# Kernel tuning notes

Measured on AMD Instinct MI355X. Metric: run time of the kernel, lower is better.

## Reference

```python
import jax, jax.numpy as jnp
import numpy as np

IGNORE_INDEX = -100


def setup_inputs() -> dict:
    key = jax.random.key(0)
    k1, k2, k3 = jax.random.split(key, 3)
    VOCAB, D = 32000, 2048
    B, S = 4, 2048
    weight = jax.random.normal(k1, (VOCAB, D), dtype=jnp.float32) * 0.02
    hidden = jax.random.normal(k2, (B, S, D), dtype=jnp.float32)
    targets = jax.random.randint(k3, (B, S), 0, VOCAB, dtype=jnp.int64)
    return {"weight": weight, "hidden": hidden, "targets": targets}


def reference(weight, hidden, targets):
    # Fused linear + cross-entropy: loss = sum_t CE(hidden_t @ W^T, target_t) / n_valid.
    # (The torch module chunks over sequence purely to save memory; the math is
    # identical to the unchunked computation below.)
    B, S, D = hidden.shape
    flat_h = hidden.reshape(-1, D)            # [B*S, D]
    flat_t = targets.reshape(-1)              # [B*S]
    logits = (flat_h @ weight.T).astype(jnp.float32)  # [B*S, V]
    lse = jax.nn.logsumexp(logits, axis=-1)   # [B*S]
    safe_t = jnp.clip(flat_t, 0, logits.shape[-1] - 1)
    tgt_logit = jnp.take_along_axis(logits, safe_t[:, None], axis=-1)[:, 0]
    valid = flat_t != IGNORE_INDEX
    per_tok = jnp.where(valid, lse - tgt_logit, 0.0)
    total_loss = per_tok.sum()
    n_valid = valid.sum().astype(jnp.float32)
    return jnp.where(n_valid > 0, total_loss / n_valid, total_loss)
```

## Files before the change

kernel.cpp:

```cpp
#include <hip/hip_runtime.h>

#define IGNORE_INDEX (-100)
#define VOCAB 32000
#define DDIM  2048
#define MTOK  8192

#define BM 128
#define BN 128
#define BK 128

#define WSCALE 32.0f
#define HSCALE 8.0f
#define INVSCALE (1.0f / 256.0f)
#define SCALE_ONE 0x7F7F7F7F

#define WBLK ((VOCAB * DDIM) / (256 * 16))
#define HBLK ((MTOK * DDIM) / (256 * 16))

typedef float f32x4 __attribute__((ext_vector_type(4)));
typedef int   i32x8 __attribute__((ext_vector_type(8)));
typedef unsigned char uchar_t;

__device__ __forceinline__ void cvt16(const float4* __restrict__ src,
                                      int4* __restrict__ dst, float scale,
                                      size_t i) {
    float4 a = src[4 * i], b = src[4 * i + 1], c = src[4 * i + 2], d = src[4 * i + 3];
    int4 o;
    int v;
    v = 0;
    v = __builtin_amdgcn_cvt_pk_fp8_f32(a.x * scale, a.y * scale, v, false);
    v = __builtin_amdgcn_cvt_pk_fp8_f32(a.z * scale, a.w * scale, v, true);
    o.x = v;
    v = 0;
    v = __builtin_amdgcn_cvt_pk_fp8_f32(b.x * scale, b.y * scale, v, false);
    v = __builtin_amdgcn_cvt_pk_fp8_f32(b.z * scale, b.w * scale, v, true);
    o.y = v;
    v = 0;
    v = __builtin_amdgcn_cvt_pk_fp8_f32(c.x * scale, c.y * scale, v, false);
    v = __builtin_amdgcn_cvt_pk_fp8_f32(c.z * scale, c.w * scale, v, true);
    o.z = v;
    v = 0;
    v = __builtin_amdgcn_cvt_pk_fp8_f32(d.x * scale, d.y * scale, v, false);
    v = __builtin_amdgcn_cvt_pk_fp8_f32(d.z * scale, d.w * scale, v, true);
    o.w = v;
    dst[i] = o;
}

__global__ void cvt_f32_fp8(const float4* __restrict__ srcW, int4* __restrict__ dstW,
                            const float4* __restrict__ srcH, int4* __restrict__ dstH) {
    if (blockIdx.x < WBLK) {
        size_t i = (size_t)blockIdx.x * blockDim.x + threadIdx.x;
        cvt16(srcW, dstW, WSCALE, i);
    } else {
        size_t i = (size_t)(blockIdx.x - WBLK) * blockDim.x + threadIdx.x;
        cvt16(srcH, dstH, HSCALE, i);
    }
}

__device__ __forceinline__ void load_lds16(const uchar_t* g, uchar_t* l) {
    __builtin_amdgcn_global_load_lds(
        (const __attribute__((address_space(1))) unsigned int*)(const void*)g,
        (__attribute__((address_space(3))) unsigned int*)(void*)l,
        16, 0, 0);
}

__global__ __launch_bounds__(256, 4) void gemm_ce(
    const uchar_t* __restrict__ A,
    const uchar_t* __restrict__ B,
    const int* __restrict__ targets,
    float* __restrict__ sumexp,
    float* __restrict__ tgtlogit) {
    __shared__ alignas(16) uchar_t As[BM * BK];
    __shared__ alignas(16) uchar_t Bs[BN * BK];

    const int tid  = threadIdx.x;
    const int wave = tid >> 6;
    const int lane = tid & 63;
    const int quad = lane >> 4;
    const int l16  = lane & 15;
    const int wm   = (wave >> 1) * 64;
    const int wn   = (wave & 1) * 64;

    const int m0 = blockIdx.x * BM;
    const int n0 = blockIdx.y * BN;

    const int srow = lane >> 3;
    const int scol = ((((lane & 7) >> 1) ^ (srow & 3)) << 5) + ((lane & 1) << 4);

    const uchar_t* Ap = A + (size_t)(m0 + wave * 32 + srow) * DDIM + scol;
    const uchar_t* Bp = B + (size_t)(n0 + wave * 32 + srow) * DDIM + scol;
    uchar_t* AsW = &As[(wave * 32) * BK];
    uchar_t* BsW = &Bs[(wave * 32) * BK];

    f32x4 acc[4][4];
    const f32x4 zero = {0.f, 0.f, 0.f, 0.f};
#pragma unroll
    for (int i = 0; i < 4; ++i)
#pragma unroll
        for (int j = 0; j < 4; ++j) acc[i][j] = zero;

#pragma clang loop unroll(disable)
    for (int k0 = 0; k0 < DDIM; k0 += BK) {
#pragma unroll
        for (int it = 0; it < 4; ++it) {
            load_lds16(Ap + (size_t)it * 8 * DDIM + k0, AsW + it * 8 * BK);
            load_lds16(Bp + (size_t)it * 8 * DDIM + k0, BsW + it * 8 * BK);
        }
        __syncthreads();

        const int gsw = ((quad ^ (l16 & 3)) << 5);
        i32x8 af[4];
#pragma unroll
        for (int i = 0; i < 4; ++i)
            af[i] = *reinterpret_cast<const i32x8*>(
                &As[(wm + i * 16 + l16) * BK + gsw]);
#pragma unroll
        for (int j = 0; j < 4; ++j) {
            const i32x8 bf = *reinterpret_cast<const i32x8*>(
                &Bs[(wn + j * 16 + l16) * BK + gsw]);
#pragma unroll
            for (int i = 0; i < 4; ++i)
                acc[i][j] = __builtin_amdgcn_mfma_scale_f32_16x16x128_f8f6f4(
                    af[i], bf, acc[i][j],
                    0 , 0 ,
                    0, SCALE_ONE, 0, SCALE_ONE);
        }
        __syncthreads();
    }

#pragma unroll
    for (int i = 0; i < 4; ++i) {
#pragma unroll
        for (int r = 0; r < 4; ++r) {
            const int mg = m0 + wm + i * 16 + quad * 4 + r;
            const int t  = targets[mg];
            float p = 0.f;
#pragma unroll
            for (int j = 0; j < 4; ++j) {
                float v = acc[i][j][r] * INVSCALE;
                p += __expf(v);
                if (t == n0 + wn + j * 16 + l16) tgtlogit[mg] = v;
            }
            p += __shfl_xor(p, 1);
            p += __shfl_xor(p, 2);
            p += __shfl_xor(p, 4);
            p += __shfl_xor(p, 8);
            if (l16 == 0) atomicAdd(&sumexp[mg], p);
        }
    }
}

__global__ void finalize(const float* __restrict__ sumexp,
                         const float* __restrict__ tgtlogit,
                         const int* __restrict__ targets,
                         float* __restrict__ out) {
    __shared__ float s_sum[8];
    __shared__ float s_cnt[8];
    float local = 0.f, cnt = 0.f;
    for (int t = threadIdx.x; t < MTOK; t += blockDim.x) {
        int tg = targets[t];
        if (tg != IGNORE_INDEX) {
            local += logf(sumexp[t]) - tgtlogit[t];
            cnt += 1.f;
        }
    }
#pragma unroll
    for (int o = 32; o > 0; o >>= 1) {
        local += __shfl_down(local, o);
        cnt   += __shfl_down(cnt, o);
    }
    const int wave = threadIdx.x >> 6, lane = threadIdx.x & 63;
    if (lane == 0) { s_sum[wave] = local; s_cnt[wave] = cnt; }
    __syncthreads();
    if (threadIdx.x == 0) {
        float ts = 0.f, tc = 0.f;
        for (int w = 0; w < (int)(blockDim.x >> 6); ++w) {
            ts += s_sum[w];
            tc += s_cnt[w];
        }
        out[0] = (tc > 0.f) ? (ts / tc) : ts;
    }
}

extern "C" void kernel_launch(void* const* d_in, const int* in_sizes, int n_in,
                              void* d_out, int out_size, void* d_ws,
                              size_t ws_size, hipStream_t stream) {
    const float* weight  = (const float*)d_in[0];
    const float* hidden  = (const float*)d_in[1];
    const int*   targets = (const int*)d_in[2];
    float* out = (float*)d_out;

    const size_t wbytes = (size_t)VOCAB * DDIM;
    const size_t hbytes = (size_t)MTOK * DDIM;
    uchar_t* Wb = (uchar_t*)d_ws;
    uchar_t* Hb = (uchar_t*)d_ws + wbytes;
    float* sumexp   = (float*)((char*)d_ws + wbytes + hbytes);
    float* tgtlogit = sumexp + MTOK;

    cvt_f32_fp8<<<WBLK + HBLK, 256, 0, stream>>>(
        (const float4*)weight, (int4*)Wb, (const float4*)hidden, (int4*)Hb);

    hipMemsetAsync(sumexp, 0, 2 * MTOK * sizeof(float), stream);

    dim3 grid(MTOK / BM, VOCAB / BN);
    gemm_ce<<<grid, 256, 0, stream>>>(Hb, Wb, targets, sumexp, tgtlogit);

    finalize<<<1, 512, 0, stream>>>(sumexp, tgtlogit, targets, out);
}
```

Baseline: 975.2 us.

## Enlarge GEMM tiles to 256x256 with double-buffered LDS and interleaved prefetch

Raises the block tile to 256x256 with 8 waves (each wave 128x64) and double-buffers the LDS, interleaving global-to-LDS prefetch of the next K tile with MFMA groups under s_setprio and explicit barriers. It also pre-reduces the per-row sum-of-exp across waves in LDS before a single atomic per row, and folds the workspace zeroing into the conversion kernel instead of a separate memset. The intent is more data reuse per loaded byte, hidden global latency, fewer atomics and one fewer launch. The trade-off is 128 KB of LDS per block, which caps occupancy at 1 block per CU despite the launch_bounds of 2, plus higher register pressure from 32 accumulators.

```diff
diff --git a/kernel.cpp b/kernel.cpp
--- a/kernel.cpp
+++ b/kernel.cpp
@@ -5,9 +5,10 @@
 #define DDIM  2048
 #define MTOK  8192
 
-#define BM 128
-#define BN 128
+#define BM 256
+#define BN 256
 #define BK 128
+#define NKT (DDIM / BK)
 
 #define WSCALE 32.0f
 #define HSCALE 8.0f
@@ -16,6 +17,7 @@
 
 #define WBLK ((VOCAB * DDIM) / (256 * 16))
 #define HBLK ((MTOK * DDIM) / (256 * 16))
+#define ZBLK ((2 * MTOK * 4) / (256 * 16))
 
 typedef float f32x4 __attribute__((ext_vector_type(4)));
 typedef int   i32x8 __attribute__((ext_vector_type(8)));
@@ -47,13 +49,17 @@
 }
 
 __global__ void cvt_f32_fp8(const float4* __restrict__ srcW, int4* __restrict__ dstW,
-                            const float4* __restrict__ srcH, int4* __restrict__ dstH) {
+                            const float4* __restrict__ srcH, int4* __restrict__ dstH,
+                            int4* __restrict__ zr) {
     if (blockIdx.x < WBLK) {
         size_t i = (size_t)blockIdx.x * blockDim.x + threadIdx.x;
         cvt16(srcW, dstW, WSCALE, i);
-    } else {
+    } else if (blockIdx.x < WBLK + HBLK) {
         size_t i = (size_t)(blockIdx.x - WBLK) * blockDim.x + threadIdx.x;
         cvt16(srcH, dstH, HSCALE, i);
+    } else {
+        int i = (blockIdx.x - WBLK - HBLK) * 256 + threadIdx.x;
+        zr[i] = make_int4(0, 0, 0, 0);
     }
 }
 
@@ -64,75 +70,135 @@
         16, 0, 0);
 }
 
-__global__ __launch_bounds__(256, 4) void gemm_ce(
+__device__ __forceinline__ i32x8 read_frag(const uchar_t* arr, int off) {
+    int4 lo = *reinterpret_cast<const int4*>(arr + off);
+    int4 hi = *reinterpret_cast<const int4*>(arr + (off ^ 16));
+    i32x8 r;
+    r[0] = lo.x; r[1] = lo.y; r[2] = lo.z; r[3] = lo.w;
+    r[4] = hi.x; r[5] = hi.y; r[6] = hi.z; r[7] = hi.w;
+    return r;
+}
+
+__global__ __launch_bounds__(512, 2) void gemm_ce(
     const uchar_t* __restrict__ A,
     const uchar_t* __restrict__ B,
     const int* __restrict__ targets,
     float* __restrict__ sumexp,
     float* __restrict__ tgtlogit) {
-    __shared__ alignas(16) uchar_t As[BM * BK];
-    __shared__ alignas(16) uchar_t Bs[BN * BK];
+    __shared__ alignas(16) uchar_t As[2][BM * BK];
+    __shared__ alignas(16) uchar_t Bs[2][BN * BK];
 
     const int tid  = threadIdx.x;
     const int wave = tid >> 6;
     const int lane = tid & 63;
     const int quad = lane >> 4;
     const int l16  = lane & 15;
-    const int wm   = (wave >> 1) * 64;
-    const int wn   = (wave & 1) * 64;
+    const int wm   = (wave >> 2) * 128;
+    const int wn   = (wave & 3) * 64;
 
     const int m0 = blockIdx.x * BM;
     const int n0 = blockIdx.y * BN;
 
     const int srow = lane >> 3;
-    const int scol = ((((lane & 7) >> 1) ^ (srow & 3)) << 5) + ((lane & 1) << 4);
-
-    const uchar_t* Ap = A + (size_t)(m0 + wave * 32 + srow) * DDIM + scol;
-    const uchar_t* Bp = B + (size_t)(n0 + wave * 32 + srow) * DDIM + scol;
-    uchar_t* AsW = &As[(wave * 32) * BK];
-    uchar_t* BsW = &Bs[(wave * 32) * BK];
-
-    f32x4 acc[4][4];
+    const int sswz = ((lane & 7) ^ srow) << 4;
+    const uchar_t* Ag = A + (size_t)(m0 + wave * 8 + srow) * DDIM + sswz;
+    const uchar_t* Bg = B + (size_t)(n0 + wave * 8 + srow) * DDIM + sswz;
+
+    const int swlo = ((quad << 1) ^ (l16 & 7)) << 4;
+    const int aoff = (wm + l16) * BK + swlo;
+    const int boff = (wn + l16) * BK + swlo;
+
+    f32x4 acc[8][4];
     const f32x4 zero = {0.f, 0.f, 0.f, 0.f};
 #pragma unroll
-    for (int i = 0; i < 4; ++i)
+    for (int i = 0; i < 8; ++i)
 #pragma unroll
         for (int j = 0; j < 4; ++j) acc[i][j] = zero;
 
+#define STAGE_A(nb, it, k0) \
+    load_lds16(Ag + (size_t)(it) * 64 * DDIM + (k0), &As[nb][(it) * 8192 + wave * 1024])
+#define STAGE_B(nb, it, k0) \
+    load_lds16(Bg + (size_t)(it) * 64 * DDIM + (k0), &Bs[nb][(it) * 8192 + wave * 1024])
+#define LGKM0 asm volatile("s_waitcnt lgkmcnt(0)" ::: "memory")
+#define VM0   asm volatile("s_waitcnt vmcnt(0)" ::: "memory")
+#define BAR   __builtin_amdgcn_s_barrier()
+
+#define MFMA_PAIR(I0)                                                          \
+    _Pragma("unroll") for (int j = 0; j < 4; ++j) {                            \
+        acc[(I0)][j] = __builtin_amdgcn_mfma_scale_f32_16x16x128_f8f6f4(       \
+            af0, bf[j], acc[(I0)][j], 0, 0, 0, SCALE_ONE, 0, SCALE_ONE);       \
+        acc[(I0) + 1][j] = __builtin_amdgcn_mfma_scale_f32_16x16x128_f8f6f4(   \
+            af1, bf[j], acc[(I0) + 1][j], 0, 0, 0, SCALE_ONE, 0, SCALE_ONE);   \
+    }
+
+#define KTILE(bufc, kt, PF)                                                    \
+    {                                                                          \
+        const uchar_t* as_ = As[bufc];                                         \
+        const uchar_t* bs_ = Bs[bufc];                                         \
+        const int kn_ = ((kt) + 1) * BK;                                       \
+        i32x8 bf[4], af0, af1;                                                 \
+                                 \
+        bf[0] = read_frag(bs_, boff);                                          \
+        bf[1] = read_frag(bs_, boff + 2048);                                   \
+        bf[2] = read_frag(bs_, boff + 4096);                                   \
+        bf[3] = read_frag(bs_, boff + 6144);                                   \
+        af0 = read_frag(as_, aoff);                                            \
+        af1 = read_frag(as_, aoff + 2048);                                     \
+        if (PF) { STAGE_A(1 - (bufc), 0, kn_); STAGE_B(1 - (bufc), 0, kn_);    \
+                  STAGE_A(1 - (bufc), 1, kn_); }                               \
+        BAR; LGKM0;                                                            \
+        __builtin_amdgcn_s_setprio(1);                                         \
+        MFMA_PAIR(0);                                                          \
+        __builtin_amdgcn_s_setprio(0);                                         \
+        BAR;                                                                   \
+                                           \
+        af0 = read_frag(as_, aoff + 2 * 2048);                                 \
+        af1 = read_frag(as_, aoff + 3 * 2048);                                 \
+        if (PF) { STAGE_B(1 - (bufc), 1, kn_); STAGE_A(1 - (bufc), 2, kn_);    \
+                  STAGE_B(1 - (bufc), 2, kn_); }                               \
+        BAR; LGKM0;                                                            \
+        __builtin_amdgcn_s_setprio(1);                                         \
+        MFMA_PAIR(2);                                                          \
+        __builtin_amdgcn_s_setprio(0);                                         \
+        BAR;                                                                   \
+                                           \
+        af0 = read_frag(as_, aoff + 4 * 2048);                                 \
+        af1 = read_frag(as_, aoff + 5 * 2048);                                 \
+        if (PF) { STAGE_A(1 - (bufc), 3, kn_); STAGE_B(1 - (bufc), 3, kn_); }  \
+        BAR; LGKM0;                                                            \
+        __builtin_amdgcn_s_setprio(1);                                         \
+        MFMA_PAIR(4);                                                          \
+        __builtin_amdgcn_s_setprio(0);                                         \
+        BAR;                                                                   \
+             \
+        af0 = read_frag(as_, aoff + 6 * 2048);                                 \
+        af1 = read_frag(as_, aoff + 7 * 2048);                                 \
+        BAR; LGKM0;                                                            \
+        __builtin_amdgcn_s_setprio(1);                                         \
+        MFMA_PAIR(6);                                                          \
+        __builtin_amdgcn_s_setprio(0);                                         \
+        VM0;                                                                   \
+        BAR;                                                                   \
+    }
+
+#pragma unroll
+    for (int it = 0; it < 4; ++it) { STAGE_A(0, it, 0); STAGE_B(0, it, 0); }
+    VM0;
+    BAR;
+
 #pragma clang loop unroll(disable)
-    for (int k0 = 0; k0 < DDIM; k0 += BK) {
-#pragma unroll
-        for (int it = 0; it < 4; ++it) {
-            load_lds16(Ap + (size_t)it * 8 * DDIM + k0, AsW + it * 8 * BK);
-            load_lds16(Bp + (size_t)it * 8 * DDIM + k0, BsW + it * 8 * BK);
-        }
-        __syncthreads();
-
-        const int gsw = ((quad ^ (l16 & 3)) << 5);
-        i32x8 af[4];
-#pragma unroll
-        for (int i = 0; i < 4; ++i)
-            af[i] = *reinterpret_cast<const i32x8*>(
-                &As[(wm + i * 16 + l16) * BK + gsw]);
-#pragma unroll
-        for (int j = 0; j < 4; ++j) {
-            const i32x8 bf = *reinterpret_cast<const i32x8*>(
-                &Bs[(wn + j * 16 + l16) * BK + gsw]);
-#pragma unroll
-            for (int i = 0; i < 4; ++i)
-                acc[i][j] = __builtin_amdgcn_mfma_scale_f32_16x16x128_f8f6f4(
-                    af[i], bf, acc[i][j],
-                    0 , 0 ,
-                    0, SCALE_ONE, 0, SCALE_ONE);
-        }
-        __syncthreads();
-    }
-
-#pragma unroll
-    for (int i = 0; i < 4; ++i) {
+    for (int kt = 0; kt < NKT; kt += 2) {
+        KTILE(0, kt, true);
+        KTILE(1, kt + 1, (kt + 1) < (NKT - 1));
+    }
+
+    float* sred = reinterpret_cast<float*>(&As[0][0]);
+#pragma unroll
+    for (int i = 0; i < 8; ++i) {
 #pragma unroll
         for (int r = 0; r < 4; ++r) {
-            const int mg = m0 + wm + i * 16 + quad * 4 + r;
+            const int rloc = wm + i * 16 + quad * 4 + r;
+            const int mg = m0 + rloc;
             const int t  = targets[mg];
             float p = 0.f;
 #pragma unroll
@@ -145,17 +211,30 @@
             p += __shfl_xor(p, 2);
             p += __shfl_xor(p, 4);
             p += __shfl_xor(p, 8);
-            if (l16 == 0) atomicAdd(&sumexp[mg], p);
+            if (l16 == 0) sred[(wave & 3) * 256 + rloc] = p;
         }
     }
+    __syncthreads();
+    if (tid < 256) {
+        float s = sred[tid] + sred[256 + tid] + sred[512 + tid] + sred[768 + tid];
+        atomicAdd(&sumexp[m0 + tid], s);
+    }
+
+#undef STAGE_A
+#undef STAGE_B
+#undef LGKM0
+#undef VM0
+#undef BAR
+#undef MFMA_PAIR
+#undef KTILE
 }
 
 __global__ void finalize(const float* __restrict__ sumexp,
                          const float* __restrict__ tgtlogit,
                          const int* __restrict__ targets,
                          float* __restrict__ out) {
-    __shared__ float s_sum[8];
-    __shared__ float s_cnt[8];
+    __shared__ float s_sum[16];
+    __shared__ float s_cnt[16];
     float local = 0.f, cnt = 0.f;
     for (int t = threadIdx.x; t < MTOK; t += blockDim.x) {
         int tg = targets[t];
@@ -197,13 +276,12 @@
     float* sumexp   = (float*)((char*)d_ws + wbytes + hbytes);
     float* tgtlogit = sumexp + MTOK;
 
-    cvt_f32_fp8<<<WBLK + HBLK, 256, 0, stream>>>(
-        (const float4*)weight, (int4*)Wb, (const float4*)hidden, (int4*)Hb);
-
-    hipMemsetAsync(sumexp, 0, 2 * MTOK * sizeof(float), stream);
+    cvt_f32_fp8<<<WBLK + HBLK + ZBLK, 256, 0, stream>>>(
+        (const float4*)weight, (int4*)Wb, (const float4*)hidden, (int4*)Hb,
+        (int4*)sumexp);
 
     dim3 grid(MTOK / BM, VOCAB / BN);
-    gemm_ce<<<grid, 256, 0, stream>>>(Hb, Wb, targets, sumexp, tgtlogit);
-
-    finalize<<<1, 512, 0, stream>>>(sumexp, tgtlogit, targets, out);
-}
+    gemm_ce<<<grid, 512, 0, stream>>>(Hb, Wb, targets, sumexp, tgtlogit);
+
+    finalize<<<1, 1024, 0, stream>>>(sumexp, tgtlogit, targets, out);
+}
```

Result: slower. 2.841 ms (+191.3%).

## Enlarge GEMM tiles to 256x256 with double-buffered LDS and interleaved prefetch

Applied to the files above, without the earlier changes.

Doubles the block tile to 256x256 with 8 waves, double-buffers LDS and spreads the next K-tile's global-to-LDS loads between MFMA groups with priority hints, to overlap memory and compute and raise reuse. The per-row exp sums are pre-reduced in shared memory so each row gets one atomic. The memset is folded into the conversion kernel. Using 128KB of LDS limits occupancy to one block per CU.

```diff
diff --git a/kernel.cpp b/kernel.cpp
--- a/kernel.cpp
+++ b/kernel.cpp
@@ -5,9 +5,10 @@
 #define DDIM  2048
 #define MTOK  8192
 
-#define BM 128
-#define BN 128
+#define BM 256
+#define BN 256
 #define BK 128
+#define NKT (DDIM / BK)
 
 #define WSCALE 32.0f
 #define HSCALE 8.0f
@@ -16,6 +17,7 @@
 
 #define WBLK ((VOCAB * DDIM) / (256 * 16))
 #define HBLK ((MTOK * DDIM) / (256 * 16))
+#define ZBLK ((2 * MTOK * 4) / (256 * 16))
 
 typedef float f32x4 __attribute__((ext_vector_type(4)));
 typedef int   i32x8 __attribute__((ext_vector_type(8)));
@@ -47,13 +49,17 @@
 }
 
 __global__ void cvt_f32_fp8(const float4* __restrict__ srcW, int4* __restrict__ dstW,
-                            const float4* __restrict__ srcH, int4* __restrict__ dstH) {
+                            const float4* __restrict__ srcH, int4* __restrict__ dstH,
+                            int4* __restrict__ zr) {
     if (blockIdx.x < WBLK) {
         size_t i = (size_t)blockIdx.x * blockDim.x + threadIdx.x;
         cvt16(srcW, dstW, WSCALE, i);
-    } else {
+    } else if (blockIdx.x < WBLK + HBLK) {
         size_t i = (size_t)(blockIdx.x - WBLK) * blockDim.x + threadIdx.x;
         cvt16(srcH, dstH, HSCALE, i);
+    } else {
+        int i = (blockIdx.x - WBLK - HBLK) * 256 + threadIdx.x;
+        zr[i] = make_int4(0, 0, 0, 0);
     }
 }
 
@@ -64,75 +70,133 @@
         16, 0, 0);
 }
 
-__global__ __launch_bounds__(256, 4) void gemm_ce(
+__device__ __forceinline__ i32x8 read_frag(const uchar_t* arr, int off) {
+    return *reinterpret_cast<const i32x8*>(arr + off);
+}
+
+__global__ __launch_bounds__(512, 2) void gemm_ce(
     const uchar_t* __restrict__ A,
     const uchar_t* __restrict__ B,
     const int* __restrict__ targets,
     float* __restrict__ sumexp,
     float* __restrict__ tgtlogit) {
-    __shared__ alignas(16) uchar_t As[BM * BK];
-    __shared__ alignas(16) uchar_t Bs[BN * BK];
+    __shared__ alignas(32) uchar_t As[2][BM * BK];
+    __shared__ alignas(32) uchar_t Bs[2][BN * BK];
 
     const int tid  = threadIdx.x;
     const int wave = tid >> 6;
     const int lane = tid & 63;
     const int quad = lane >> 4;
     const int l16  = lane & 15;
-    const int wm   = (wave >> 1) * 64;
-    const int wn   = (wave & 1) * 64;
+    const int wm   = (wave >> 2) * 128;
+    const int wn   = (wave & 3) * 64;
 
     const int m0 = blockIdx.x * BM;
     const int n0 = blockIdx.y * BN;
 
     const int srow = lane >> 3;
     const int scol = ((((lane & 7) >> 1) ^ (srow & 3)) << 5) + ((lane & 1) << 4);
-
-    const uchar_t* Ap = A + (size_t)(m0 + wave * 32 + srow) * DDIM + scol;
-    const uchar_t* Bp = B + (size_t)(n0 + wave * 32 + srow) * DDIM + scol;
-    uchar_t* AsW = &As[(wave * 32) * BK];
-    uchar_t* BsW = &Bs[(wave * 32) * BK];
-
-    f32x4 acc[4][4];
+    const uchar_t* Ag = A + (size_t)(m0 + wave * 32 + srow) * DDIM + scol;
+    const uchar_t* Bg = B + (size_t)(n0 + wave * 32 + srow) * DDIM + scol;
+
+    const int gsw  = (quad ^ (l16 & 3)) << 5;
+    const int aoff = (wm + l16) * BK + gsw;
+    const int boff = (wn + l16) * BK + gsw;
+
+    f32x4 acc[8][4];
     const f32x4 zero = {0.f, 0.f, 0.f, 0.f};
 #pragma unroll
-    for (int i = 0; i < 4; ++i)
+    for (int i = 0; i < 8; ++i)
 #pragma unroll
         for (int j = 0; j < 4; ++j) acc[i][j] = zero;
 
+#define BAR    asm volatile("s_barrier" ::: "memory")
+#define SCHED0 __builtin_amdgcn_sched_barrier(0)
+#define PRIO1  __builtin_amdgcn_s_setprio(1)
+#define PRIO0  __builtin_amdgcn_s_setprio(0)
+#define VM0    asm volatile("s_waitcnt vmcnt(0)" ::: "memory")
+
+#define MFMA2(I, a0, a1)                                                       \
+    _Pragma("unroll") for (int j_ = 0; j_ < 4; ++j_) {                         \
+        acc[(I)][j_] = __builtin_amdgcn_mfma_scale_f32_16x16x128_f8f6f4(       \
+            a0, bfr[j_], acc[(I)][j_], 0, 0, 0, SCALE_ONE, 0, SCALE_ONE);      \
+        acc[(I) + 1][j_] = __builtin_amdgcn_mfma_scale_f32_16x16x128_f8f6f4(   \
+            a1, bfr[j_], acc[(I) + 1][j_], 0, 0, 0, SCALE_ONE, 0, SCALE_ONE);  \
+    }
+
+    {
+        uchar_t* a_ = &As[0][0] + (wave * 32) * BK;
+        uchar_t* b_ = &Bs[0][0] + (wave * 32) * BK;
+#pragma unroll
+        for (int it = 0; it < 4; ++it) {
+            load_lds16(Ag + (size_t)it * 8 * DDIM, a_ + it * 8 * BK);
+            load_lds16(Bg + (size_t)it * 8 * DDIM, b_ + it * 8 * BK);
+        }
+    }
+    VM0;
+    BAR;
+
 #pragma clang loop unroll(disable)
-    for (int k0 = 0; k0 < DDIM; k0 += BK) {
-#pragma unroll
-        for (int it = 0; it < 4; ++it) {
-            load_lds16(Ap + (size_t)it * 8 * DDIM + k0, AsW + it * 8 * BK);
-            load_lds16(Bp + (size_t)it * 8 * DDIM + k0, BsW + it * 8 * BK);
-        }
-        __syncthreads();
-
-        const int gsw = ((quad ^ (l16 & 3)) << 5);
-        i32x8 af[4];
-#pragma unroll
-        for (int i = 0; i < 4; ++i)
-            af[i] = *reinterpret_cast<const i32x8*>(
-                &As[(wm + i * 16 + l16) * BK + gsw]);
-#pragma unroll
-        for (int j = 0; j < 4; ++j) {
-            const i32x8 bf = *reinterpret_cast<const i32x8*>(
-                &Bs[(wn + j * 16 + l16) * BK + gsw]);
-#pragma unroll
-            for (int i = 0; i < 4; ++i)
-                acc[i][j] = __builtin_amdgcn_mfma_scale_f32_16x16x128_f8f6f4(
-                    af[i], bf, acc[i][j],
-                    0 , 0 ,
-                    0, SCALE_ONE, 0, SCALE_ONE);
-        }
-        __syncthreads();
-    }
-
-#pragma unroll
-    for (int i = 0; i < 4; ++i) {
+    for (int t = 0; t < NKT; ++t) {
+        const uchar_t* as_ = &As[t & 1][0];
+        const uchar_t* bs_ = &Bs[t & 1][0];
+        uchar_t* an_ = &As[(t + 1) & 1][0] + (wave * 32) * BK;
+        uchar_t* bn_ = &Bs[(t + 1) & 1][0] + (wave * 32) * BK;
+        const int kn = (t + 1) * BK;
+        const bool pf = (t < NKT - 1);
+        i32x8 bfr[4], af0, af1;
+
+#pragma unroll
+        for (int j = 0; j < 4; ++j) bfr[j] = read_frag(bs_, boff + j * 2048);
+        af0 = read_frag(as_, aoff);
+        af1 = read_frag(as_, aoff + 2048);
+        if (pf) {
+            load_lds16(Ag + kn, an_);
+            load_lds16(Ag + 8 * DDIM + kn, an_ + 8 * BK);
+            load_lds16(Bg + kn, bn_);
+        }
+        BAR; SCHED0; PRIO1;
+        MFMA2(0, af0, af1);
+        PRIO0; BAR;
+
+        af0 = read_frag(as_, aoff + 2 * 2048);
+        af1 = read_frag(as_, aoff + 3 * 2048);
+        if (pf) {
+            load_lds16(Ag + 16 * DDIM + kn, an_ + 16 * BK);
+            load_lds16(Ag + 24 * DDIM + kn, an_ + 24 * BK);
+            load_lds16(Bg + 8 * DDIM + kn, bn_ + 8 * BK);
+        }
+        BAR; SCHED0; PRIO1;
+        MFMA2(2, af0, af1);
+        PRIO0; BAR;
+
+        af0 = read_frag(as_, aoff + 4 * 2048);
+        af1 = read_frag(as_, aoff + 5 * 2048);
+        if (pf) {
+            load_lds16(Bg + 16 * DDIM + kn, bn_ + 16 * BK);
+            load_lds16(Bg + 24 * DDIM + kn, bn_ + 24 * BK);
+        }
+        BAR; SCHED0; PRIO1;
+        MFMA2(4, af0, af1);
+        PRIO0; BAR;
+
+        af0 = read_frag(as_, aoff + 6 * 2048);
+        af1 = read_frag(as_, aoff + 7 * 2048);
+        BAR; SCHED0; PRIO1;
+        MFMA2(6, af0, af1);
+        PRIO0;
+        VM0;
+        BAR;
+    }
+
+    __syncthreads();
+    float* sred = reinterpret_cast<float*>(&As[0][0]);
+#pragma unroll
+    for (int i = 0; i < 8; ++i) {
 #pragma unroll
         for (int r = 0; r < 4; ++r) {
-            const int mg = m0 + wm + i * 16 + quad * 4 + r;
+            const int rloc = wm + i * 16 + quad * 4 + r;
+            const int mg = m0 + rloc;
             const int t  = targets[mg];
             float p = 0.f;
 #pragma unroll
@@ -145,17 +209,29 @@
             p += __shfl_xor(p, 2);
             p += __shfl_xor(p, 4);
             p += __shfl_xor(p, 8);
-            if (l16 == 0) atomicAdd(&sumexp[mg], p);
-        }
-    }
+            if (l16 == 0) sred[(wave & 3) * 256 + rloc] = p;
+        }
+    }
+    __syncthreads();
+    if (tid < 256) {
+        float s = sred[tid] + sred[256 + tid] + sred[512 + tid] + sred[768 + tid];
+        atomicAdd(&sumexp[m0 + tid], s);
+    }
+
+#undef BAR
+#undef SCHED0
+#undef PRIO1
+#undef PRIO0
+#undef VM0
+#undef MFMA2
 }
 
 __global__ void finalize(const float* __restrict__ sumexp,
                          const float* __restrict__ tgtlogit,
                          const int* __restrict__ targets,
                          float* __restrict__ out) {
-    __shared__ float s_sum[8];
-    __shared__ float s_cnt[8];
+    __shared__ float s_sum[16];
+    __shared__ float s_cnt[16];
     float local = 0.f, cnt = 0.f;
     for (int t = threadIdx.x; t < MTOK; t += blockDim.x) {
         int tg = targets[t];
@@ -197,13 +273,12 @@
     float* sumexp   = (float*)((char*)d_ws + wbytes + hbytes);
     float* tgtlogit = sumexp + MTOK;
 
-    cvt_f32_fp8<<<WBLK + HBLK, 256, 0, stream>>>(
-        (const float4*)weight, (int4*)Wb, (const float4*)hidden, (int4*)Hb);
-
-    hipMemsetAsync(sumexp, 0, 2 * MTOK * sizeof(float), stream);
+    cvt_f32_fp8<<<WBLK + HBLK + ZBLK, 256, 0, stream>>>(
+        (const float4*)weight, (int4*)Wb, (const float4*)hidden, (int4*)Hb,
+        (int4*)sumexp);
 
     dim3 grid(MTOK / BM, VOCAB / BN);
-    gemm_ce<<<grid, 256, 0, stream>>>(Hb, Wb, targets, sumexp, tgtlogit);
-
-    finalize<<<1, 512, 0, stream>>>(sumexp, tgtlogit, targets, out);
-}
+    gemm_ce<<<grid, 512, 0, stream>>>(Hb, Wb, targets, sumexp, tgtlogit);
+
+    finalize<<<1, 1024, 0, stream>>>(sumexp, tgtlogit, targets, out);
+}
```

New measurement: 1.123 ms. 1.15x slower.
